# Performance work log

Hardware: AMD Instinct MI355X
Metric: run time of the kernel (lower is better)

The kernel has to match this reference:

```python
import jax, jax.numpy as jnp
import numpy as np

B, N, D, E, H = 2, 50000, 64, 800000, 32


def setup_inputs() -> dict:
    key = jax.random.key(0)
    ks = jax.random.split(key, 17)
    u = lambda k, shape: jax.random.uniform(k, shape, minval=-0.01, maxval=0.01, dtype=jnp.float32)
    return {
        "x_state": jax.random.uniform(ks[0], (B, N, 1), dtype=jnp.float32),
        "x_influence": jax.random.normal(ks[1], (B, N, D), dtype=jnp.float32),
        "L_indices": jax.random.randint(ks[2], (E, 2), 0, N, dtype=jnp.int32),
        "L_values": jax.random.uniform(ks[3], (E,), dtype=jnp.float32),
        "self_activation": jax.random.normal(ks[4], (N, 1), dtype=jnp.float32) * 0.01,
        "Xs": jax.random.uniform(ks[5], (B, N, 1), dtype=jnp.float32),
        "weight_trans": u(ks[6], (D, D)),
        "state_beta": u(ks[7], (2 * D, 1)),
        "state_weight_self": u(ks[8], ()),
        "state_weight_neighbor": u(ks[9], ()),
        "sg_w1": u(ks[10], (1, H)),
        "sg_b1": u(ks[11], (1, H)),
        "sg_w2": u(ks[12], (H, 1)),
        "sg_b2": u(ks[13], (1, 1)),
        "influence_attention": u(ks[14], (2 * D, 1)),
        "influence_weight_self": u(ks[15], ()),
        "influence_weight_neighbor": u(ks[16], ()),
    }


def _segsum(x, ids, n):
    return jax.ops.segment_sum(x, ids, num_segments=n)


def reference(x_state, x_influence, L_indices, L_values, self_activation, Xs,
              weight_trans, state_beta, state_weight_self, state_weight_neighbor,
              sg_w1, sg_b1, sg_w2, sg_b2,
              influence_attention, influence_weight_self, influence_weight_neighbor):
    b, n, d = x_influence.shape
    row = L_indices[:, 0]
    col = L_indices[:, 1]

    # linear transform of influence features: [B, N, D]
    tf_feat = jnp.einsum('bnd,de->bne', x_influence, weight_trans)

    # ---- state branch: per-edge leaky-relu attention (alpha=0.02), no softmax ----
    # concat([row_repre, col_repre]) @ beta == row_repre @ beta[:D] + col_repre @ beta[D:]
    s_r = tf_feat @ state_beta[:d, 0]   # [B, N]
    s_c = tf_feat @ state_beta[d:, 0]   # [B, N]
    logit_s = jax.nn.leaky_relu(s_r[:, row] + s_c[:, col], negative_slope=0.02)  # [B, E]
    msg_s = logit_s * x_state[:, col, 0]                                          # [B, E]
    S_neigh = _segsum(msg_s.T, row, n).T[:, :, None] + self_activation[None]      # [B, N, 1]
    S_update = jax.nn.elu(state_weight_self * x_state + state_weight_neighbor * S_neigh)
    output_state = S_update * (1.0 - Xs) + Xs

    # ---- state gating MLP: elu(elu(x @ w1 + b1) @ w2 + b2) ----
    xs = x_state.reshape(-1, 1)
    gate = jax.nn.elu(jax.nn.elu(xs @ sg_w1 + sg_b1) @ sg_w2 + sg_b2).reshape(b, n, 1)
    filt = tf_feat * gate  # [B, N, D]

    # ---- influence branch: leaky-relu (alpha=0.2) attention + sparse softmax per row ----
    e_r = tf_feat @ influence_attention[:d, 0]
    e_c = tf_feat @ influence_attention[d:, 0]
    logit_e = jax.nn.leaky_relu(e_r[:, row] + e_c[:, col], negative_slope=0.2).T  # [E, B]
    m = jax.ops.segment_max(logit_e, row, num_segments=n)                          # [N, B]
    ex = jnp.exp(logit_e - m[row])
    den = _segsum(ex, row, n)                                                      # [N, B]
    soft = ex / den[row]                                                           # [E, B]
    msg_e = soft[:, :, None] * jnp.transpose(filt[:, col, :], (1, 0, 2))           # [E, B, D]
    E_neigh = jnp.transpose(_segsum(msg_e, row, n), (1, 0, 2))                     # [B, N, D]
    output_influence = jax.nn.elu(influence_weight_self * tf_feat
                                  + influence_weight_neighbor * E_neigh)
    return (output_state, output_influence)
```

## Files before the change

### kernel.cpp

```cpp
#include <hip/hip_runtime.h>
#include <math.h>


#define CAP 64

__device__ __forceinline__ float elu_f(float x) {
    return x > 0.f ? x : __expf(x) - 1.f;
}
__device__ __forceinline__ unsigned short f2bf(float f) {
    unsigned u = __float_as_uint(f);
    return (unsigned short)((u + 0x7fffu + ((u >> 16) & 1u)) >> 16);
}
__device__ __forceinline__ float bf2f(unsigned short h) {
    return __uint_as_float(((unsigned)h) << 16);
}

__global__ __launch_bounds__(256) void k_gemm(
    const float* __restrict__ x_infl, const float* __restrict__ Wg,
    unsigned short* __restrict__ tf16, int BN)
{
    __shared__ float4 xs4[1024];
    int tid = threadIdx.x;
    int lane = tid & 63;

    float wcol[64];
#pragma unroll
    for (int k = 0; k < 64; ++k) wcol[k] = Wg[k * 64 + lane];

    size_t gbase = (size_t)blockIdx.x * 1024;
    size_t gmax = (size_t)BN * 16 - 1;
    const float4* xg = (const float4*)x_infl;
#pragma unroll
    for (int q = 0; q < 4; ++q) {
        size_t g = gbase + q * 256 + tid;
        xs4[q * 256 + tid] = xg[g > gmax ? gmax : g];
    }
    __syncthreads();

    int wrow = (tid >> 6) * 16;
    int r0 = blockIdx.x * 64;
    for (int rp = 0; rp < 8; ++rp) {
        int ra = wrow + rp * 2;
        float acca = 0.f, accb = 0.f;
#pragma unroll
        for (int k4 = 0; k4 < 16; ++k4) {
            float4 va = xs4[ra * 16 + k4];
            float4 vb = xs4[ra * 16 + 16 + k4];
            acca = fmaf(va.x, wcol[4 * k4 + 0], acca);
            acca = fmaf(va.y, wcol[4 * k4 + 1], acca);
            acca = fmaf(va.z, wcol[4 * k4 + 2], acca);
            acca = fmaf(va.w, wcol[4 * k4 + 3], acca);
            accb = fmaf(vb.x, wcol[4 * k4 + 0], accb);
            accb = fmaf(vb.y, wcol[4 * k4 + 1], accb);
            accb = fmaf(vb.z, wcol[4 * k4 + 2], accb);
            accb = fmaf(vb.w, wcol[4 * k4 + 3], accb);
        }
        int g0 = r0 + ra, g1 = g0 + 1;
        if (g0 < BN) tf16[((size_t)g0 << 6) + lane] = f2bf(acca);
        if (g1 < BN) tf16[((size_t)g1 << 6) + lane] = f2bf(accb);
    }
}

__global__ __launch_bounds__(256) void k_nd(
    const float* __restrict__ x_infl, const float* __restrict__ Wg,
    const float* __restrict__ sbeta, const float* __restrict__ iatt,
    const float* __restrict__ x_state,
    const float* __restrict__ w1, const float* __restrict__ b1,
    const float* __restrict__ w2, const float* __restrict__ b2,
    float4* __restrict__ node4, float2* __restrict__ rpack, int BN)
{
    __shared__ float4 b4[64], wb4[64];
    int tid = threadIdx.x;
    if (tid < 64)
        b4[tid] = make_float4(sbeta[tid], sbeta[64 + tid],
                              iatt[tid], iatt[64 + tid]);
    __syncthreads();
    if (tid < 64) {
        const float* wr = Wg + tid * 64;
        float asr = 0.f, asc = 0.f, aer = 0.f, aec = 0.f;
#pragma unroll
        for (int j = 0; j < 64; ++j) {
            float w = wr[j]; float4 bb = b4[j];
            asr = fmaf(w, bb.x, asr); asc = fmaf(w, bb.y, asc);
            aer = fmaf(w, bb.z, aer); aec = fmaf(w, bb.w, aec);
        }
        wb4[tid] = make_float4(asr, asc, aer, aec);
    }
    __syncthreads();

    int r = blockIdx.x * 256 + tid;
    int rr = (r < BN) ? r : BN - 1;
    const float4* xr = (const float4*)(x_infl + ((size_t)rr << 6));
    float sr = 0.f, sc = 0.f, er = 0.f, ec = 0.f;
#pragma unroll
    for (int k4 = 0; k4 < 16; ++k4) {
        float4 xv = xr[k4];
        float4 u0 = wb4[4 * k4 + 0], u1 = wb4[4 * k4 + 1];
        float4 u2 = wb4[4 * k4 + 2], u3 = wb4[4 * k4 + 3];
        sr = fmaf(xv.x, u0.x, sr); sc = fmaf(xv.x, u0.y, sc);
        er = fmaf(xv.x, u0.z, er); ec = fmaf(xv.x, u0.w, ec);
        sr = fmaf(xv.y, u1.x, sr); sc = fmaf(xv.y, u1.y, sc);
        er = fmaf(xv.y, u1.z, er); ec = fmaf(xv.y, u1.w, ec);
        sr = fmaf(xv.z, u2.x, sr); sc = fmaf(xv.z, u2.y, sc);
        er = fmaf(xv.z, u2.z, er); ec = fmaf(xv.z, u2.w, ec);
        sr = fmaf(xv.w, u3.x, sr); sc = fmaf(xv.w, u3.y, sc);
        er = fmaf(xv.w, u3.z, er); ec = fmaf(xv.w, u3.w, ec);
    }

    float xs = x_state[rr];
    float tacc = b2[0];
#pragma unroll
    for (int h = 0; h < 32; ++h)
        tacc = fmaf(elu_f(fmaf(xs, w1[h], b1[h])), w2[h], tacc);
    float gate = elu_f(tacc);

    if (r < BN) {
        node4[r] = make_float4(ec, sc, xs, gate);
        rpack[r] = make_float2(er, sr);
    }
}

__global__ __launch_bounds__(256) void k_bucket(const int2* __restrict__ Li,
                                                int* __restrict__ counts,
                                                unsigned short* __restrict__ bcols,
                                                int E) {
    int e = blockIdx.x * 256 + threadIdx.x;
    if (e < E) {
        int2 rc = Li[e];
        int p = atomicAdd(&counts[rc.x], 1);
        if (p < CAP) bcols[rc.x * CAP + p] = (unsigned short)rc.y;
    }
}

__global__ __launch_bounds__(256) void k_row(
    const int* __restrict__ counts, const unsigned short* __restrict__ bcols,
    const unsigned short* __restrict__ tf16, const float4* __restrict__ node4,
    const float2* __restrict__ rpack,
    const float* __restrict__ x_state, const float* __restrict__ self_act,
    const float* __restrict__ Xs,
    const float* __restrict__ sws_p, const float* __restrict__ swn_p,
    const float* __restrict__ iws_p, const float* __restrict__ iwn_p,
    float* __restrict__ out_state, float* __restrict__ out_infl, int N)
{
    int lane = threadIdx.x & 63;
    int n = blockIdx.x * 4 + __builtin_amdgcn_readfirstlane(threadIdx.x >> 6);

    int cnt = counts[n];
    cnt = (cnt > CAP) ? CAP : cnt;

    float2 rp0 = rpack[n];
    float2 rp1 = rpack[N + n];
    const unsigned short* tfb0 = tf16;
    const unsigned short* tfb1 = tf16 + ((size_t)N << 6);

    float tsel0 = bf2f(tfb0[((size_t)n << 6) + lane]);
    float tsel1 = bf2f(tfb1[((size_t)n << 6) + lane]);

    float lsum0 = 0.f, lsum1 = 0.f, sacc0 = 0.f, sacc1 = 0.f;
    float acc0[8], acc1[8];
#pragma unroll
    for (int j = 0; j < 8; ++j) { acc0[j] = 0.f; acc1[j] = 0.f; }

    if (cnt > 0) {
        bool act = lane < cnt;
        int c = bcols[n * CAP + (act ? lane : 0)];
        float4 ns0 = node4[c];
        float4 ns1 = node4[N + c];

        float lgs0 = rp0.y + ns0.y;
        lgs0 = (lgs0 > 0.f) ? lgs0 : 0.02f * lgs0;
        sacc0 = act ? lgs0 * ns0.z : 0.f;
        float lg0 = rp0.x + ns0.x;
        lg0 = (lg0 > 0.f) ? lg0 : 0.2f * lg0;
        float pp0 = act ? __expf(lg0) : 0.f;
        lsum0 = pp0;
        float wgt0 = pp0 * ns0.w;

        float lgs1 = rp1.y + ns1.y;
        lgs1 = (lgs1 > 0.f) ? lgs1 : 0.02f * lgs1;
        sacc1 = act ? lgs1 * ns1.z : 0.f;
        float lg1 = rp1.x + ns1.x;
        lg1 = (lg1 > 0.f) ? lg1 : 0.2f * lg1;
        float pp1 = act ? __expf(lg1) : 0.f;
        lsum1 = pp1;
        float wgt1 = pp1 * ns1.w;

        unsigned pkA = ((unsigned)f2bf(wgt0) << 16) | (unsigned)c;
        unsigned pkB = ((unsigned)f2bf(wgt1) << 16) | (unsigned)c;

        int cnt8 = (cnt + 7) & ~7;
        for (int k = 0; k < cnt8; k += 8) {
#pragma unroll
            for (int j = 0; j < 8; ++j) {
                unsigned pA = (unsigned)__builtin_amdgcn_readlane((int)pkA, k + j);
                unsigned pB = (unsigned)__builtin_amdgcn_readlane((int)pkB, k + j);
                size_t off = ((size_t)(pA & 0xffffu) << 6) + lane;
                float w0 = __uint_as_float(pA & 0xffff0000u);
                float w1 = __uint_as_float(pB & 0xffff0000u);
                acc0[j] = fmaf(w0, bf2f(tfb0[off]), acc0[j]);
                acc1[j] = fmaf(w1, bf2f(tfb1[off]), acc1[j]);
            }
        }
    }
    float accA = (((acc0[0] + acc0[1]) + (acc0[2] + acc0[3])) +
                  ((acc0[4] + acc0[5]) + (acc0[6] + acc0[7])));
    float accB = (((acc1[0] + acc1[1]) + (acc1[2] + acc1[3])) +
                  ((acc1[4] + acc1[5]) + (acc1[6] + acc1[7])));

#pragma unroll
    for (int m = 1; m < 64; m <<= 1) {
        lsum0 += __shfl_xor(lsum0, m, 64);
        lsum1 += __shfl_xor(lsum1, m, 64);
        sacc0 += __shfl_xor(sacc0, m, 64);
        sacc1 += __shfl_xor(sacc1, m, 64);
    }

    float En0 = (cnt > 0) ? accA / lsum0 : 0.f;
    float En1 = (cnt > 0) ? accB / lsum1 : 0.f;

    float iws = iws_p[0], iwn = iwn_p[0];
    out_infl[((size_t)n << 6) + lane]       = elu_f(fmaf(iwn, En0, iws * tsel0));
    out_infl[((size_t)(N + n) << 6) + lane] = elu_f(fmaf(iwn, En1, iws * tsel1));

    if (lane == 0) {
        float sws = sws_p[0], swn = swn_p[0];
        float sa = self_act[n];

        float Sn0 = sacc0 + sa;
        float su0 = elu_f(fmaf(swn, Sn0, sws * x_state[n]));
        float X0 = Xs[n];
        out_state[n] = fmaf(su0, 1.f - X0, X0);

        float Sn1 = sacc1 + sa;
        float su1 = elu_f(fmaf(swn, Sn1, sws * x_state[N + n]));
        float X1 = Xs[N + n];
        out_state[N + n] = fmaf(su1, 1.f - X1, X1);
    }
}

extern "C" void kernel_launch(void* const* d_in, const int* in_sizes, int n_in,
                              void* d_out, int out_size, void* d_ws, size_t ws_size,
                              hipStream_t stream) {
    const float* x_state  = (const float*)d_in[0];
    const float* x_infl   = (const float*)d_in[1];
    const int*   L_ind    = (const int*)d_in[2];
    const float* self_act = (const float*)d_in[4];
    const float* Xs       = (const float*)d_in[5];
    const float* Wg       = (const float*)d_in[6];
    const float* sbeta    = (const float*)d_in[7];
    const float* sws      = (const float*)d_in[8];
    const float* swn      = (const float*)d_in[9];
    const float* w1       = (const float*)d_in[10];
    const float* b1       = (const float*)d_in[11];
    const float* w2       = (const float*)d_in[12];
    const float* b2       = (const float*)d_in[13];
    const float* iatt     = (const float*)d_in[14];
    const float* iws      = (const float*)d_in[15];
    const float* iwn      = (const float*)d_in[16];

    const int N  = in_sizes[4];
    const int BN = in_sizes[0];
    const int E  = in_sizes[2] / 2;

    char* p = (char*)d_ws;
    auto alloc = [&](size_t bytes) {
        void* q = (void*)p;
        p += (bytes + 255) & ~(size_t)255;
        return q;
    };
    unsigned short* tf16  = (unsigned short*)alloc((size_t)BN * 64 * 2);
    float4*         node4 = (float4*)alloc((size_t)BN * 16);
    float2*         rpack = (float2*)alloc((size_t)BN * 8);
    int*            counts = (int*)  alloc((size_t)N * 4);
    unsigned short* bcols = (unsigned short*)alloc((size_t)N * CAP * 2);

    hipMemsetAsync(counts, 0, (size_t)N * 4, stream);

    k_bucket<<<(E + 255) / 256, 256, 0, stream>>>((const int2*)L_ind,
                                                  counts, bcols, E);

    k_gemm<<<(BN + 63) / 64, 256, 0, stream>>>(x_infl, Wg, tf16, BN);

    k_nd<<<(BN + 255) / 256, 256, 0, stream>>>(x_infl, Wg, sbeta, iatt,
                                               x_state, w1, b1, w2, b2,
                                               node4, rpack, BN);

    k_row<<<N / 4, 256, 0, stream>>>(counts, bcols, tf16, node4, rpack,
                                     x_state, self_act, Xs,
                                     sws, swn, iws, iwn,
                                     (float*)d_out, (float*)d_out + BN, N);
}
```

Before: 230.3 us.

## Fuse bucketing, GEMM and node-projection kernels into one interleaved launch

Merges the edge bucketing, the bf16 tf GEMM and the per-node attention/gate kernels into a single launch. Block indices are interleaved in groups of 13 (8 bucket, 4 GEMM, 1 node), so the atomic-heavy bucketing runs alongside the compute and bandwidth-bound work. This removes two launch gaps and lets the three independent stages overlap. In exchange, every block now carries the register and shared-memory footprint of the heaviest branch, which can lower occupancy for the light bucketing blocks.

```diff
diff --git a/kernel.cpp b/kernel.cpp
--- a/kernel.cpp
+++ b/kernel.cpp
@@ -15,120 +15,131 @@
     return __uint_as_float(((unsigned)h) << 16);
 }
 
-__global__ __launch_bounds__(256) void k_gemm(
+__global__ __launch_bounds__(256) void k_fused(
+    const int2* __restrict__ Li, int* __restrict__ counts,
+    unsigned short* __restrict__ bcols, int E, int nb_b,
     const float* __restrict__ x_infl, const float* __restrict__ Wg,
-    unsigned short* __restrict__ tf16, int BN)
-{
-    __shared__ float4 xs4[1024];
-    int tid = threadIdx.x;
-    int lane = tid & 63;
-
-    float wcol[64];
-#pragma unroll
-    for (int k = 0; k < 64; ++k) wcol[k] = Wg[k * 64 + lane];
-
-    size_t gbase = (size_t)blockIdx.x * 1024;
-    size_t gmax = (size_t)BN * 16 - 1;
-    const float4* xg = (const float4*)x_infl;
-#pragma unroll
-    for (int q = 0; q < 4; ++q) {
-        size_t g = gbase + q * 256 + tid;
-        xs4[q * 256 + tid] = xg[g > gmax ? gmax : g];
-    }
-    __syncthreads();
-
-    int wrow = (tid >> 6) * 16;
-    int r0 = blockIdx.x * 64;
-    for (int rp = 0; rp < 8; ++rp) {
-        int ra = wrow + rp * 2;
-        float acca = 0.f, accb = 0.f;
-#pragma unroll
-        for (int k4 = 0; k4 < 16; ++k4) {
-            float4 va = xs4[ra * 16 + k4];
-            float4 vb = xs4[ra * 16 + 16 + k4];
-            acca = fmaf(va.x, wcol[4 * k4 + 0], acca);
-            acca = fmaf(va.y, wcol[4 * k4 + 1], acca);
-            acca = fmaf(va.z, wcol[4 * k4 + 2], acca);
-            acca = fmaf(va.w, wcol[4 * k4 + 3], acca);
-            accb = fmaf(vb.x, wcol[4 * k4 + 0], accb);
-            accb = fmaf(vb.y, wcol[4 * k4 + 1], accb);
-            accb = fmaf(vb.z, wcol[4 * k4 + 2], accb);
-            accb = fmaf(vb.w, wcol[4 * k4 + 3], accb);
-        }
-        int g0 = r0 + ra, g1 = g0 + 1;
-        if (g0 < BN) tf16[((size_t)g0 << 6) + lane] = f2bf(acca);
-        if (g1 < BN) tf16[((size_t)g1 << 6) + lane] = f2bf(accb);
-    }
-}
-
-__global__ __launch_bounds__(256) void k_nd(
-    const float* __restrict__ x_infl, const float* __restrict__ Wg,
+    unsigned short* __restrict__ tf16, int BN, int nb_g,
     const float* __restrict__ sbeta, const float* __restrict__ iatt,
     const float* __restrict__ x_state,
     const float* __restrict__ w1, const float* __restrict__ b1,
     const float* __restrict__ w2, const float* __restrict__ b2,
-    float4* __restrict__ node4, float2* __restrict__ rpack, int BN)
+    float4* __restrict__ node4, float2* __restrict__ rpack, int nb_n)
 {
-    __shared__ float4 b4[64], wb4[64];
+    __shared__ float4 xs4[1024];
     int tid = threadIdx.x;
-    if (tid < 64)
-        b4[tid] = make_float4(sbeta[tid], sbeta[64 + tid],
-                              iatt[tid], iatt[64 + tid]);
-    __syncthreads();
-    if (tid < 64) {
-        const float* wr = Wg + tid * 64;
-        float asr = 0.f, asc = 0.f, aer = 0.f, aec = 0.f;
-#pragma unroll
-        for (int j = 0; j < 64; ++j) {
-            float w = wr[j]; float4 bb = b4[j];
-            asr = fmaf(w, bb.x, asr); asc = fmaf(w, bb.y, asc);
-            aer = fmaf(w, bb.z, aer); aec = fmaf(w, bb.w, aec);
-        }
-        wb4[tid] = make_float4(asr, asc, aer, aec);
-    }
-    __syncthreads();
-
-    int r = blockIdx.x * 256 + tid;
-    int rr = (r < BN) ? r : BN - 1;
-    const float4* xr = (const float4*)(x_infl + ((size_t)rr << 6));
-    float sr = 0.f, sc = 0.f, er = 0.f, ec = 0.f;
-#pragma unroll
-    for (int k4 = 0; k4 < 16; ++k4) {
-        float4 xv = xr[k4];
-        float4 u0 = wb4[4 * k4 + 0], u1 = wb4[4 * k4 + 1];
-        float4 u2 = wb4[4 * k4 + 2], u3 = wb4[4 * k4 + 3];
-        sr = fmaf(xv.x, u0.x, sr); sc = fmaf(xv.x, u0.y, sc);
-        er = fmaf(xv.x, u0.z, er); ec = fmaf(xv.x, u0.w, ec);
-        sr = fmaf(xv.y, u1.x, sr); sc = fmaf(xv.y, u1.y, sc);
-        er = fmaf(xv.y, u1.z, er); ec = fmaf(xv.y, u1.w, ec);
-        sr = fmaf(xv.z, u2.x, sr); sc = fmaf(xv.z, u2.y, sc);
-        er = fmaf(xv.z, u2.z, er); ec = fmaf(xv.z, u2.w, ec);
-        sr = fmaf(xv.w, u3.x, sr); sc = fmaf(xv.w, u3.y, sc);
-        er = fmaf(xv.w, u3.z, er); ec = fmaf(xv.w, u3.w, ec);
-    }
-
-    float xs = x_state[rr];
-    float tacc = b2[0];
-#pragma unroll
-    for (int h = 0; h < 32; ++h)
-        tacc = fmaf(elu_f(fmaf(xs, w1[h], b1[h])), w2[h], tacc);
-    float gate = elu_f(tacc);
-
-    if (r < BN) {
-        node4[r] = make_float4(ec, sc, xs, gate);
-        rpack[r] = make_float2(er, sr);
-    }
-}
-
-__global__ __launch_bounds__(256) void k_bucket(const int2* __restrict__ Li,
-                                                int* __restrict__ counts,
-                                                unsigned short* __restrict__ bcols,
-                                                int E) {
-    int e = blockIdx.x * 256 + threadIdx.x;
-    if (e < E) {
-        int2 rc = Li[e];
-        int p = atomicAdd(&counts[rc.x], 1);
-        if (p < CAP) bcols[rc.x * CAP + p] = (unsigned short)rc.y;
+    int bid = blockIdx.x;
+    int per = bid / 13, q = bid % 13;
+
+    if (q < 8) {
+        int idx = per * 8 + q;
+        if (idx >= nb_b) return;
+        int e = idx * 256 + tid;
+        if (e < E) {
+            int2 rc = Li[e];
+            int p = atomicAdd(&counts[rc.x], 1);
+            if (p < CAP) bcols[rc.x * CAP + p] = (unsigned short)rc.y;
+        }
+        return;
+    }
+
+    if (q < 12) {
+        int idx = per * 4 + (q - 8);
+        if (idx >= nb_g) return;
+        int lane = tid & 63;
+
+        float wcol[64];
+#pragma unroll
+        for (int k = 0; k < 64; ++k) wcol[k] = Wg[k * 64 + lane];
+
+        size_t gbase = (size_t)idx * 1024;
+        size_t gmax = (size_t)BN * 16 - 1;
+        const float4* xg = (const float4*)x_infl;
+#pragma unroll
+        for (int u = 0; u < 4; ++u) {
+            size_t g = gbase + u * 256 + tid;
+            xs4[u * 256 + tid] = xg[g > gmax ? gmax : g];
+        }
+        __syncthreads();
+
+        int wrow = (tid >> 6) * 16;
+        int r0 = idx * 64;
+        for (int rp = 0; rp < 8; ++rp) {
+            int ra = wrow + rp * 2;
+            float acca = 0.f, accb = 0.f;
+#pragma unroll
+            for (int k4 = 0; k4 < 16; ++k4) {
+                float4 va = xs4[ra * 16 + k4];
+                float4 vb = xs4[ra * 16 + 16 + k4];
+                acca = fmaf(va.x, wcol[4 * k4 + 0], acca);
+                acca = fmaf(va.y, wcol[4 * k4 + 1], acca);
+                acca = fmaf(va.z, wcol[4 * k4 + 2], acca);
+                acca = fmaf(va.w, wcol[4 * k4 + 3], acca);
+                accb = fmaf(vb.x, wcol[4 * k4 + 0], accb);
+                accb = fmaf(vb.y, wcol[4 * k4 + 1], accb);
+                accb = fmaf(vb.z, wcol[4 * k4 + 2], accb);
+                accb = fmaf(vb.w, wcol[4 * k4 + 3], accb);
+            }
+            int g0 = r0 + ra, g1 = g0 + 1;
+            if (g0 < BN) tf16[((size_t)g0 << 6) + lane] = f2bf(acca);
+            if (g1 < BN) tf16[((size_t)g1 << 6) + lane] = f2bf(accb);
+        }
+        return;
+    }
+
+    {
+        int idx = per;
+        if (idx >= nb_n) return;
+        float4* b4  = xs4;
+        float4* wb4 = xs4 + 64;
+
+        if (tid < 64)
+            b4[tid] = make_float4(sbeta[tid], sbeta[64 + tid],
+                                  iatt[tid], iatt[64 + tid]);
+        __syncthreads();
+        if (tid < 64) {
+            const float* wr = Wg + tid * 64;
+            float asr = 0.f, asc = 0.f, aer = 0.f, aec = 0.f;
+#pragma unroll
+            for (int j = 0; j < 64; ++j) {
+                float w = wr[j]; float4 bb = b4[j];
+                asr = fmaf(w, bb.x, asr); asc = fmaf(w, bb.y, asc);
+                aer = fmaf(w, bb.z, aer); aec = fmaf(w, bb.w, aec);
+            }
+            wb4[tid] = make_float4(asr, asc, aer, aec);
+        }
+        __syncthreads();
+
+        int r = idx * 256 + tid;
+        int rr = (r < BN) ? r : BN - 1;
+        const float4* xr = (const float4*)(x_infl + ((size_t)rr << 6));
+        float sr = 0.f, sc = 0.f, er = 0.f, ec = 0.f;
+#pragma unroll
+        for (int k4 = 0; k4 < 16; ++k4) {
+            float4 xv = xr[k4];
+            float4 u0 = wb4[4 * k4 + 0], u1 = wb4[4 * k4 + 1];
+            float4 u2 = wb4[4 * k4 + 2], u3 = wb4[4 * k4 + 3];
+            sr = fmaf(xv.x, u0.x, sr); sc = fmaf(xv.x, u0.y, sc);
+            er = fmaf(xv.x, u0.z, er); ec = fmaf(xv.x, u0.w, ec);
+            sr = fmaf(xv.y, u1.x, sr); sc = fmaf(xv.y, u1.y, sc);
+            er = fmaf(xv.y, u1.z, er); ec = fmaf(xv.y, u1.w, ec);
+            sr = fmaf(xv.z, u2.x, sr); sc = fmaf(xv.z, u2.y, sc);
+            er = fmaf(xv.z, u2.z, er); ec = fmaf(xv.z, u2.w, ec);
+            sr = fmaf(xv.w, u3.x, sr); sc = fmaf(xv.w, u3.y, sc);
+            er = fmaf(xv.w, u3.z, er); ec = fmaf(xv.w, u3.w, ec);
+        }
+
+        float xs = x_state[rr];
+        float tacc = b2[0];
+#pragma unroll
+        for (int h = 0; h < 32; ++h)
+            tacc = fmaf(elu_f(fmaf(xs, w1[h], b1[h])), w2[h], tacc);
+        float gate = elu_f(tacc);
+
+        if (r < BN) {
+            node4[r] = make_float4(ec, sc, xs, gate);
+            rpack[r] = make_float2(er, sr);
+        }
     }
 }
 
@@ -276,14 +287,18 @@
 
     hipMemsetAsync(counts, 0, (size_t)N * 4, stream);
 
-    k_bucket<<<(E + 255) / 256, 256, 0, stream>>>((const int2*)L_ind,
-                                                  counts, bcols, E);
-
-    k_gemm<<<(BN + 63) / 64, 256, 0, stream>>>(x_infl, Wg, tf16, BN);
-
-    k_nd<<<(BN + 255) / 256, 256, 0, stream>>>(x_infl, Wg, sbeta, iatt,
-                                               x_state, w1, b1, w2, b2,
-                                               node4, rpack, BN);
+    const int nb_b = (E + 255) / 256;
+    const int nb_g = (BN + 63) / 64;
+    const int nb_n = (BN + 255) / 256;
+    int P = (nb_b + 7) / 8;
+    int Pg = (nb_g + 3) / 4; if (Pg > P) P = Pg;
+    if (nb_n > P) P = nb_n;
+
+    k_fused<<<13 * P, 256, 0, stream>>>((const int2*)L_ind, counts, bcols,
+                                        E, nb_b,
+                                        x_infl, Wg, tf16, BN, nb_g,
+                                        sbeta, iatt, x_state,
+                                        w1, b1, w2, b2, node4, rpack, nb_n);
 
     k_row<<<N / 4, 256, 0, stream>>>(counts, bcols, tf16, node4, rpack,
                                      x_state, self_act, Xs,
```

Result: faster. 191.0 us (-17.1%).
